# Optimization experiments

Measured on AMD Instinct MI355X. Metric: run time of the kernel, lower is better.

Reference implementation:

```python
import jax, jax.numpy as jnp
import numpy as np

B, T, D_IN, D_OUT, N_HEAD = 2, 2048, 1024, 1024, 16
HEAD_DIM = D_OUT // N_HEAD


def setup_inputs() -> dict:
    key = jax.random.key(0)
    k1, k2, k3, k4 = jax.random.split(key, 4)
    s = 0.02  # init scale for weights
    return {
        "x": jax.random.normal(k1, (B, T, D_IN), jnp.float32),
        "Wq": jax.random.normal(k2, (D_OUT, D_IN), jnp.float32) * s,
        "Wk": jax.random.normal(k3, (D_OUT, D_IN), jnp.float32) * s,
        "Wv": jax.random.normal(k4, (D_OUT, D_IN), jnp.float32) * s,
    }


def reference(x, Wq, Wk, Wv):
    b, t, _ = x.shape
    h, hd = N_HEAD, HEAD_DIM
    # Linear projections (torch Linear: x @ W.T), split heads -> [b,h,t,hd]
    q = (x @ Wq.T).reshape(b, t, h, hd).transpose(0, 2, 1, 3)
    k = (x @ Wk.T).reshape(b, t, h, hd).transpose(0, 2, 1, 3)
    v = (x @ Wv.T).reshape(b, t, h, hd).transpose(0, 2, 1, 3)
    # raw scores [b,h,t,t], causal mask BEFORE scaling (as in source)
    omega = jnp.einsum("bhqd,bhkd->bhqk", q, k)
    causal = jnp.triu(jnp.ones((t, t), dtype=bool), k=1)
    omega = jnp.where(causal, -jnp.inf, omega)
    attw = jax.nn.softmax(omega / jnp.sqrt(jnp.asarray(hd, omega.dtype)), axis=-1)
    ctx = jnp.einsum("bhqk,bhkd->bhqd", attw, v)  # [b,h,t,hd]
    # Faithful to source: transpose(2,3) then view(B,T,d_out)
    out = jnp.swapaxes(ctx, 2, 3).reshape(b, t, D_OUT)
    return out
```

## Files before the change

### kernel.cpp

```cpp
#include <hip/hip_runtime.h>
#include <hip/hip_bf16.h>
#include <stdint.h>

typedef __attribute__((ext_vector_type(8))) short s16x8;
typedef __attribute__((ext_vector_type(4))) float f32x4;

#define T_   2048
#define NH   16
#define HD   64
#define DIN  1024
#define SCALE_LOG2 0.18033688011112042f

#define MFMA32(a, b, c) __builtin_amdgcn_mfma_f32_16x16x32_bf16(a, b, c, 0, 0, 0)

__device__ __forceinline__ unsigned short f2bf(float f) {
  union { float f; uint32_t u; } c; c.f = f;
  uint32_t u = c.u;
  return (unsigned short)((u + 0x7FFFu + ((u >> 16) & 1u)) >> 16);
}

__device__ __forceinline__ uint32_t pk_bf16(float a, float b) {
  __hip_bfloat162 h = __float22bfloat162_rn(make_float2(a, b));
  return *reinterpret_cast<uint32_t*>(&h);
}

#define GLL(gp, lp) __builtin_amdgcn_global_load_lds( \
    (__attribute__((address_space(1))) void*)(gp),    \
    (__attribute__((address_space(3))) void*)(lp), 16, 0, 0)

__global__ __launch_bounds__(256) void cvt_kernel(
    const float* __restrict__ x,  const float* __restrict__ wq,
    const float* __restrict__ wk, const float* __restrict__ wv,
    unsigned short* __restrict__ xb, unsigned short* __restrict__ wb) {
  int i = (blockIdx.x * 256 + threadIdx.x) * 4;
  float4 v;
  unsigned short* dp;
  if (i < 4194304) {
    v = *(const float4*)(x + i);
    dp = xb + i;
  } else {
    int j = i - 4194304;
    int seg = j >> 20, r = j & 1048575;
    const float* w = (seg == 0) ? wq : (seg == 1) ? wk : wv;
    v = *(const float4*)(w + r);
    dp = wb + j;
  }
  ushort4 o;
  o.x = f2bf(v.x); o.y = f2bf(v.y); o.z = f2bf(v.z); o.w = f2bf(v.w);
  *(ushort4*)dp = o;
}

__global__ __launch_bounds__(256) void qkv_gemm(
    const unsigned short* __restrict__ A, const unsigned short* __restrict__ Bm,
    unsigned short* __restrict__ qkv) {
  __shared__ __attribute__((aligned(16))) unsigned short Alds[64 * 64];
  __shared__ __attribute__((aligned(16))) unsigned short Blds[128 * 64];
  const int tid = threadIdx.x;
  const int lane = tid & 63, wave = tid >> 6;
  const int wm = wave >> 1, wn = wave & 1;
  const int m0 = blockIdx.y * 64, n0 = blockIdx.x * 128;

  f32x4 acc[2][4] = {};

  const int srA = wave * 16 + (lane >> 3);
  const int srB = wave * 32 + (lane >> 3);
  const int scol = (((lane & 7) ^ ((lane >> 3) & 7))) * 8;
  const unsigned short* ag = A  + (size_t)(m0 + srA) * DIN + scol;
  const unsigned short* bg = Bm + (size_t)(n0 + srB) * DIN + scol;
  unsigned short* al = &Alds[wave * 16 * 64];
  unsigned short* bl = &Blds[wave * 32 * 64];

  const int l16 = lane & 15, quad = lane >> 4;
  const int sw = l16 & 7;

  for (int k0 = 0; k0 < DIN; k0 += 64) {
    __syncthreads();
#pragma unroll
    for (int i = 0; i < 2; i++)
      GLL(ag + (size_t)i * 8 * DIN + k0, al + i * 512);
#pragma unroll
    for (int i = 0; i < 4; i++)
      GLL(bg + (size_t)i * 8 * DIN + k0, bl + i * 512);
    __syncthreads();
#pragma unroll
    for (int ks = 0; ks < 2; ks++) {
      const int cl = ((ks * 4 + quad) ^ sw) * 8;
      s16x8 af[2], bf[4];
#pragma unroll
      for (int mt = 0; mt < 2; mt++)
        af[mt] = *(const s16x8*)&Alds[(wm * 32 + mt * 16 + l16) * 64 + cl];
#pragma unroll
      for (int nt = 0; nt < 4; nt++)
        bf[nt] = *(const s16x8*)&Blds[(wn * 64 + nt * 16 + l16) * 64 + cl];
#pragma unroll
      for (int mt = 0; mt < 2; mt++)
#pragma unroll
        for (int nt = 0; nt < 4; nt++)
          acc[mt][nt] = MFMA32(af[mt], bf[nt], acc[mt][nt]);
    }
  }

#pragma unroll
  for (int mt = 0; mt < 2; mt++) {
    int mbase = m0 + wm * 32 + mt * 16 + (quad << 2);
    int b = mbase >> 11, t = mbase & 2047;
#pragma unroll
    for (int nt = 0; nt < 4; nt++) {
      int n = n0 + wn * 64 + nt * 16 + l16;
      int sel = n >> 10, h = (n >> 6) & 15, d = n & 63;
      int bh = b * NH + h;
      if (sel == 2) {
        ushort4 pk;
        pk.x = f2bf(acc[mt][nt][0]); pk.y = f2bf(acc[mt][nt][1]);
        pk.z = f2bf(acc[mt][nt][2]); pk.w = f2bf(acc[mt][nt][3]);
        *(ushort4*)&qkv[8388608 + (size_t)(bh * HD + d) * T_ + t] = pk;
      } else {
        float qs = (sel == 0) ? SCALE_LOG2 : 1.f;
#pragma unroll
        for (int r = 0; r < 4; r++)
          qkv[(size_t)sel * 4194304 + (size_t)(bh * T_ + t + r) * HD + d] =
              f2bf(acc[mt][nt][r] * qs);
      }
    }
  }
}

__global__ __launch_bounds__(256) void attn_kernel(
    const unsigned short* __restrict__ qkv, float* __restrict__ out) {
  __shared__ __attribute__((aligned(16))) unsigned short Klds[64 * 64];
  __shared__ __attribute__((aligned(16))) unsigned short Vt[64 * 64];
  __shared__ __attribute__((aligned(16))) unsigned short Plds[64 * 64];

  const int lane = threadIdx.x & 63, wave = threadIdx.x >> 6;
  const int l16 = lane & 15, quad = lane >> 4;
  const int swl = l16 & 7;
  const int qt = 31 - blockIdx.y, bh = blockIdx.x;
  const int q0 = qt * 64;
  const size_t bh_off = (size_t)bh * (T_ * HD);
  const unsigned short* Q  = qkv + bh_off;
  const unsigned short* Kb = qkv + 4194304 + bh_off;
  const unsigned short* Vb = qkv + 8388608 + bh_off;

  s16x8 qf[2];
  {
    const unsigned short* qp =
        Q + (size_t)(q0 + wave * 16 + l16) * HD + quad * 8;
    qf[0] = *(const s16x8*)(qp);
    qf[1] = *(const s16x8*)(qp + 32);
  }

  const int sr = threadIdx.x >> 3;
  const int sc = (threadIdx.x & 7) * 8;
  const int swc = (((threadIdx.x & 7) ^ (sr & 7))) * 8;

  s16x8 kr0 = *(const s16x8*)&Kb[(size_t)sr * HD + sc];
  s16x8 kr1 = *(const s16x8*)&Kb[(size_t)(sr + 32) * HD + sc];
  s16x8 vr0 = *(const s16x8*)&Vb[(size_t)sr * T_ + sc];
  s16x8 vr1 = *(const s16x8*)&Vb[(size_t)(sr + 32) * T_ + sc];

  const s16x8 onesf = {0x3F80, 0x3F80, 0x3F80, 0x3F80,
                       0x3F80, 0x3F80, 0x3F80, 0x3F80};
  f32x4 o[4] = {};
  f32x4 lacc = {};

  uint32_t* prow = (uint32_t*)&Plds[(wave * 16 + l16) * 64];
  const unsigned short* prd = &Plds[(wave * 16 + l16) * 64];

  for (int kt = 0; kt <= qt; kt++) {
    __syncthreads();
    *(s16x8*)&Klds[sr * 64 + swc] = kr0;
    *(s16x8*)&Klds[(sr + 32) * 64 + swc] = kr1;
    *(s16x8*)&Vt[sr * 64 + swc] = vr0;
    *(s16x8*)&Vt[(sr + 32) * 64 + swc] = vr1;
    if (kt < qt) {
      const unsigned short* kp = Kb + (size_t)(kt + 1) * 64 * HD;
      const unsigned short* vp = Vb + (kt + 1) * 64;
      kr0 = *(const s16x8*)&kp[(size_t)sr * HD + sc];
      kr1 = *(const s16x8*)&kp[(size_t)(sr + 32) * HD + sc];
      vr0 = *(const s16x8*)&vp[(size_t)sr * T_ + sc];
      vr1 = *(const s16x8*)&vp[(size_t)(sr + 32) * T_ + sc];
    }
    __syncthreads();

    f32x4 s[4] = {};
#pragma unroll
    for (int kk = 0; kk < 2; kk++) {
      const int cl = ((kk * 4 + quad) ^ swl) * 8;
#pragma unroll
      for (int nt = 0; nt < 4; nt++) {
        s16x8 kf = *(const s16x8*)&Klds[(nt * 16 + l16) * 64 + cl];
        s[nt] = MFMA32(kf, qf[kk], s[nt]);
      }
    }

    if (kt < qt) {
#pragma unroll
      for (int nt = 0; nt < 4; nt++) {
        float p0 = exp2f(s[nt][0]);
        float p1 = exp2f(s[nt][1]);
        float p2 = exp2f(s[nt][2]);
        float p3 = exp2f(s[nt][3]);
        *(uint2*)&prow[(((2 * nt + (quad >> 1)) ^ swl) << 2) + (quad & 1) * 2] =
            make_uint2(pk_bf16(p0, p1), pk_bf16(p2, p3));
      }
    } else {
      const int lim = wave * 16 + l16;
#pragma unroll
      for (int nt = 0; nt < 4; nt++) {
        const int kb = nt * 16 + quad * 4;
        float p0 = (kb + 0 <= lim) ? exp2f(s[nt][0]) : 0.f;
        float p1 = (kb + 1 <= lim) ? exp2f(s[nt][1]) : 0.f;
        float p2 = (kb + 2 <= lim) ? exp2f(s[nt][2]) : 0.f;
        float p3 = (kb + 3 <= lim) ? exp2f(s[nt][3]) : 0.f;
        *(uint2*)&prow[(((2 * nt + (quad >> 1)) ^ swl) << 2) + (quad & 1) * 2] =
            make_uint2(pk_bf16(p0, p1), pk_bf16(p2, p3));
      }
    }

#pragma unroll
    for (int kk = 0; kk < 2; kk++) {
      const int cl = ((kk * 4 + quad) ^ swl) * 8;
      s16x8 pf = *(const s16x8*)&prd[cl];
      lacc = MFMA32(pf, onesf, lacc);
#pragma unroll
      for (int dt = 0; dt < 4; dt++) {
        s16x8 vf = *(const s16x8*)&Vt[(dt * 16 + l16) * 64 + cl];
        o[dt] = MFMA32(pf, vf, o[dt]);
      }
    }
  }

  f32x4 inv;
#pragma unroll
  for (int r = 0; r < 4; r++) inv[r] = 1.f / lacc[r];
#pragma unroll
  for (int dt = 0; dt < 4; dt++) {
    float4 v = make_float4(o[dt][0] * inv[0], o[dt][1] * inv[1],
                           o[dt][2] * inv[2], o[dt][3] * inv[3]);
    *(float4*)(out + (size_t)bh * (HD * T_) + (size_t)(dt * 16 + l16) * T_ +
               q0 + wave * 16 + quad * 4) = v;
  }
}

extern "C" void kernel_launch(void* const* d_in, const int* in_sizes, int n_in,
                              void* d_out, int out_size, void* d_ws, size_t ws_size,
                              hipStream_t stream) {
  const float* x  = (const float*)d_in[0];
  const float* wq = (const float*)d_in[1];
  const float* wk = (const float*)d_in[2];
  const float* wv = (const float*)d_in[3];
  float* out = (float*)d_out;

  unsigned short* xb  = (unsigned short*)d_ws;
  unsigned short* wb  = xb + 4194304;
  unsigned short* qkv = wb + 3145728;

  cvt_kernel<<<7168, 256, 0, stream>>>(x, wq, wk, wv, xb, wb);
  dim3 g1(24, 64);
  qkv_gemm<<<g1, 256, 0, stream>>>(xb, wb, qkv);
  dim3 g2(32, 32);
  attn_kernel<<<g2, 256, 0, stream>>>(qkv, out);
}
```

Measured before the change: 147.3 us.

## Use two waves per 32 query rows with double-buffered direct-to-LDS K/V loads

The attention block drops from four waves to two. Each wave now owns 32 query rows (two 16-row tiles), so every K and V fragment read from LDS feeds two MFMAs. The register-staged K/V prefetch is replaced by asynchronous global-to-LDS loads into a double-buffered K/V tile, which removes one barrier per iteration. In exchange the kernel has fewer waves per block, uses more registers per wave, and relies on the barrier to make the async loads visible before use.

```diff
diff --git a/kernel.cpp b/kernel.cpp
--- a/kernel.cpp
+++ b/kernel.cpp
@@ -125,10 +125,10 @@
   }
 }
 
-__global__ __launch_bounds__(256) void attn_kernel(
+__global__ __launch_bounds__(128) void attn_kernel(
     const unsigned short* __restrict__ qkv, float* __restrict__ out) {
-  __shared__ __attribute__((aligned(16))) unsigned short Klds[64 * 64];
-  __shared__ __attribute__((aligned(16))) unsigned short Vt[64 * 64];
+  __shared__ __attribute__((aligned(16))) unsigned short Klds[2][64 * 64];
+  __shared__ __attribute__((aligned(16))) unsigned short Vt[2][64 * 64];
   __shared__ __attribute__((aligned(16))) unsigned short Plds[64 * 64];
 
   const int lane = threadIdx.x & 63, wave = threadIdx.x >> 6;
@@ -141,104 +141,127 @@
   const unsigned short* Kb = qkv + 4194304 + bh_off;
   const unsigned short* Vb = qkv + 8388608 + bh_off;
 
-  s16x8 qf[2];
-  {
+  s16x8 qf[2][2];
+#pragma unroll
+  for (int nt = 0; nt < 2; nt++) {
     const unsigned short* qp =
-        Q + (size_t)(q0 + wave * 16 + l16) * HD + quad * 8;
-    qf[0] = *(const s16x8*)(qp);
-    qf[1] = *(const s16x8*)(qp + 32);
-  }
-
-  const int sr = threadIdx.x >> 3;
-  const int sc = (threadIdx.x & 7) * 8;
-  const int swc = (((threadIdx.x & 7) ^ (sr & 7))) * 8;
-
-  s16x8 kr0 = *(const s16x8*)&Kb[(size_t)sr * HD + sc];
-  s16x8 kr1 = *(const s16x8*)&Kb[(size_t)(sr + 32) * HD + sc];
-  s16x8 vr0 = *(const s16x8*)&Vb[(size_t)sr * T_ + sc];
-  s16x8 vr1 = *(const s16x8*)&Vb[(size_t)(sr + 32) * T_ + sc];
+        Q + (size_t)(q0 + wave * 32 + nt * 16 + l16) * HD + quad * 8;
+    qf[nt][0] = *(const s16x8*)(qp);
+    qf[nt][1] = *(const s16x8*)(qp + 32);
+  }
+
+  const int r8 = lane >> 3;
+  const int xc = ((lane & 7) ^ r8) * 8;
+  const unsigned short* kg = Kb + (size_t)(wave * 32 + r8) * HD + xc;
+  const unsigned short* vg = Vb + (size_t)(wave * 32 + r8) * T_ + xc;
+  const int sbase = wave * 32 * 64;
 
   const s16x8 onesf = {0x3F80, 0x3F80, 0x3F80, 0x3F80,
                        0x3F80, 0x3F80, 0x3F80, 0x3F80};
-  f32x4 o[4] = {};
-  f32x4 lacc = {};
-
-  uint32_t* prow = (uint32_t*)&Plds[(wave * 16 + l16) * 64];
-  const unsigned short* prd = &Plds[(wave * 16 + l16) * 64];
-
+  f32x4 o[2][4] = {};
+  f32x4 lacc[2] = {};
+
+#pragma unroll
+  for (int i = 0; i < 4; i++) {
+    GLL(kg + (size_t)i * 8 * HD, &Klds[0][sbase + i * 8 * 64]);
+    GLL(vg + (size_t)i * 8 * T_, &Vt[0][sbase + i * 8 * 64]);
+  }
+
+  int cur = 0;
   for (int kt = 0; kt <= qt; kt++) {
     __syncthreads();
-    *(s16x8*)&Klds[sr * 64 + swc] = kr0;
-    *(s16x8*)&Klds[(sr + 32) * 64 + swc] = kr1;
-    *(s16x8*)&Vt[sr * 64 + swc] = vr0;
-    *(s16x8*)&Vt[(sr + 32) * 64 + swc] = vr1;
     if (kt < qt) {
-      const unsigned short* kp = Kb + (size_t)(kt + 1) * 64 * HD;
-      const unsigned short* vp = Vb + (kt + 1) * 64;
-      kr0 = *(const s16x8*)&kp[(size_t)sr * HD + sc];
-      kr1 = *(const s16x8*)&kp[(size_t)(sr + 32) * HD + sc];
-      vr0 = *(const s16x8*)&vp[(size_t)sr * T_ + sc];
-      vr1 = *(const s16x8*)&vp[(size_t)(sr + 32) * T_ + sc];
-    }
-    __syncthreads();
-
-    f32x4 s[4] = {};
+      const unsigned short* kp = kg + (size_t)(kt + 1) * 64 * HD;
+      const unsigned short* vp = vg + (kt + 1) * 64;
+      unsigned short* kd = &Klds[cur ^ 1][sbase];
+      unsigned short* vd = &Vt[cur ^ 1][sbase];
+#pragma unroll
+      for (int i = 0; i < 4; i++) {
+        GLL(kp + (size_t)i * 8 * HD, kd + i * 8 * 64);
+        GLL(vp + (size_t)i * 8 * T_, vd + i * 8 * 64);
+      }
+    }
+
+    f32x4 s[4][2] = {};
 #pragma unroll
     for (int kk = 0; kk < 2; kk++) {
       const int cl = ((kk * 4 + quad) ^ swl) * 8;
 #pragma unroll
-      for (int nt = 0; nt < 4; nt++) {
-        s16x8 kf = *(const s16x8*)&Klds[(nt * 16 + l16) * 64 + cl];
-        s[nt] = MFMA32(kf, qf[kk], s[nt]);
+      for (int mt = 0; mt < 4; mt++) {
+        s16x8 kf = *(const s16x8*)&Klds[cur][(mt * 16 + l16) * 64 + cl];
+#pragma unroll
+        for (int nt = 0; nt < 2; nt++)
+          s[mt][nt] = MFMA32(kf, qf[nt][kk], s[mt][nt]);
       }
     }
 
     if (kt < qt) {
 #pragma unroll
-      for (int nt = 0; nt < 4; nt++) {
-        float p0 = exp2f(s[nt][0]);
-        float p1 = exp2f(s[nt][1]);
-        float p2 = exp2f(s[nt][2]);
-        float p3 = exp2f(s[nt][3]);
-        *(uint2*)&prow[(((2 * nt + (quad >> 1)) ^ swl) << 2) + (quad & 1) * 2] =
-            make_uint2(pk_bf16(p0, p1), pk_bf16(p2, p3));
+      for (int nt = 0; nt < 2; nt++) {
+        uint32_t* prow = (uint32_t*)&Plds[(wave * 32 + nt * 16 + l16) * 64];
+#pragma unroll
+        for (int mt = 0; mt < 4; mt++) {
+          float p0 = exp2f(s[mt][nt][0]);
+          float p1 = exp2f(s[mt][nt][1]);
+          float p2 = exp2f(s[mt][nt][2]);
+          float p3 = exp2f(s[mt][nt][3]);
+          *(uint2*)&prow[(((2 * mt + (quad >> 1)) ^ swl) << 2) +
+                         (quad & 1) * 2] =
+              make_uint2(pk_bf16(p0, p1), pk_bf16(p2, p3));
+        }
       }
     } else {
-      const int lim = wave * 16 + l16;
-#pragma unroll
-      for (int nt = 0; nt < 4; nt++) {
-        const int kb = nt * 16 + quad * 4;
-        float p0 = (kb + 0 <= lim) ? exp2f(s[nt][0]) : 0.f;
-        float p1 = (kb + 1 <= lim) ? exp2f(s[nt][1]) : 0.f;
-        float p2 = (kb + 2 <= lim) ? exp2f(s[nt][2]) : 0.f;
-        float p3 = (kb + 3 <= lim) ? exp2f(s[nt][3]) : 0.f;
-        *(uint2*)&prow[(((2 * nt + (quad >> 1)) ^ swl) << 2) + (quad & 1) * 2] =
-            make_uint2(pk_bf16(p0, p1), pk_bf16(p2, p3));
+#pragma unroll
+      for (int nt = 0; nt < 2; nt++) {
+        const int lim = wave * 32 + nt * 16 + l16;
+        uint32_t* prow = (uint32_t*)&Plds[(wave * 32 + nt * 16 + l16) * 64];
+#pragma unroll
+        for (int mt = 0; mt < 4; mt++) {
+          const int kb = mt * 16 + quad * 4;
+          float p0 = (kb + 0 <= lim) ? exp2f(s[mt][nt][0]) : 0.f;
+          float p1 = (kb + 1 <= lim) ? exp2f(s[mt][nt][1]) : 0.f;
+          float p2 = (kb + 2 <= lim) ? exp2f(s[mt][nt][2]) : 0.f;
+          float p3 = (kb + 3 <= lim) ? exp2f(s[mt][nt][3]) : 0.f;
+          *(uint2*)&prow[(((2 * mt + (quad >> 1)) ^ swl) << 2) +
+                         (quad & 1) * 2] =
+              make_uint2(pk_bf16(p0, p1), pk_bf16(p2, p3));
+        }
       }
     }
 
 #pragma unroll
     for (int kk = 0; kk < 2; kk++) {
       const int cl = ((kk * 4 + quad) ^ swl) * 8;
-      s16x8 pf = *(const s16x8*)&prd[cl];
-      lacc = MFMA32(pf, onesf, lacc);
+      s16x8 pf[2];
+#pragma unroll
+      for (int nt = 0; nt < 2; nt++) {
+        pf[nt] =
+            *(const s16x8*)&Plds[(wave * 32 + nt * 16 + l16) * 64 + cl];
+        lacc[nt] = MFMA32(pf[nt], onesf, lacc[nt]);
+      }
 #pragma unroll
       for (int dt = 0; dt < 4; dt++) {
-        s16x8 vf = *(const s16x8*)&Vt[(dt * 16 + l16) * 64 + cl];
-        o[dt] = MFMA32(pf, vf, o[dt]);
-      }
-    }
-  }
-
-  f32x4 inv;
-#pragma unroll
-  for (int r = 0; r < 4; r++) inv[r] = 1.f / lacc[r];
-#pragma unroll
-  for (int dt = 0; dt < 4; dt++) {
-    float4 v = make_float4(o[dt][0] * inv[0], o[dt][1] * inv[1],
-                           o[dt][2] * inv[2], o[dt][3] * inv[3]);
-    *(float4*)(out + (size_t)bh * (HD * T_) + (size_t)(dt * 16 + l16) * T_ +
-               q0 + wave * 16 + quad * 4) = v;
+        s16x8 vf = *(const s16x8*)&Vt[cur][(dt * 16 + l16) * 64 + cl];
+#pragma unroll
+        for (int nt = 0; nt < 2; nt++)
+          o[nt][dt] = MFMA32(pf[nt], vf, o[nt][dt]);
+      }
+    }
+    cur ^= 1;
+  }
+
+#pragma unroll
+  for (int nt = 0; nt < 2; nt++) {
+    f32x4 inv;
+#pragma unroll
+    for (int r = 0; r < 4; r++) inv[r] = 1.f / lacc[nt][r];
+#pragma unroll
+    for (int dt = 0; dt < 4; dt++) {
+      float4 v = make_float4(o[nt][dt][0] * inv[0], o[nt][dt][1] * inv[1],
+                             o[nt][dt][2] * inv[2], o[nt][dt][3] * inv[3]);
+      *(float4*)(out + (size_t)bh * (HD * T_) + (size_t)(dt * 16 + l16) * T_ +
+                 q0 + wave * 32 + nt * 16 + quad * 4) = v;
+    }
   }
 }
 
@@ -259,5 +282,5 @@
   dim3 g1(24, 64);
   qkv_gemm<<<g1, 256, 0, stream>>>(xb, wb, qkv);
   dim3 g2(32, 32);
-  attn_kernel<<<g2, 256, 0, stream>>>(qkv, out);
-}
+  attn_kernel<<<g2, 128, 0, stream>>>(qkv, out);
+}
```

After: 166.5 us. +13.1%, slower.

## Pair causal query tiles per block to balance attention workload

Applied to the files above, without the earlier changes.

Each attention block now processes two query tiles, a long one (qa = 31-qb) and a short one (qb), streaming the needed K/V tiles for both in a single 33-iteration loop. The grid is halved accordingly. This aims to remove the causal load imbalance where late blocks run 32 tiles and early blocks run 1. In exchange it uses more registers for two sets of accumulators and Q fragments, and has half as many blocks, which could reduce occupancy or latency hiding.

```diff
diff --git a/kernel.cpp b/kernel.cpp
--- a/kernel.cpp
+++ b/kernel.cpp
@@ -125,56 +125,118 @@
   }
 }
 
+__device__ __forceinline__ void tile_step(
+    const unsigned short* Klds, const unsigned short* Vt,
+    unsigned short* Plds, const s16x8 qf0, const s16x8 qf1,
+    f32x4 o[4], f32x4& lacc,
+    const int l16, const int quad, const int swl, const int wave,
+    const bool diag) {
+  f32x4 s[4] = {};
+#pragma unroll
+  for (int kk = 0; kk < 2; kk++) {
+    const int cl = ((kk * 4 + quad) ^ swl) * 8;
+    const s16x8 q = kk ? qf1 : qf0;
+#pragma unroll
+    for (int mt = 0; mt < 4; mt++) {
+      s16x8 kf = *(const s16x8*)&Klds[(mt * 16 + l16) * 64 + cl];
+      s[mt] = MFMA32(kf, q, s[mt]);
+    }
+  }
+
+  uint32_t* prow = (uint32_t*)&Plds[(wave * 16 + l16) * 64];
+  if (!diag) {
+#pragma unroll
+    for (int mt = 0; mt < 4; mt++) {
+      float p0 = exp2f(s[mt][0]);
+      float p1 = exp2f(s[mt][1]);
+      float p2 = exp2f(s[mt][2]);
+      float p3 = exp2f(s[mt][3]);
+      *(uint2*)&prow[(((2 * mt + (quad >> 1)) ^ swl) << 2) + (quad & 1) * 2] =
+          make_uint2(pk_bf16(p0, p1), pk_bf16(p2, p3));
+    }
+  } else {
+    const int lim = wave * 16 + l16;
+#pragma unroll
+    for (int mt = 0; mt < 4; mt++) {
+      const int kb = mt * 16 + quad * 4;
+      float p0 = (kb + 0 <= lim) ? exp2f(s[mt][0]) : 0.f;
+      float p1 = (kb + 1 <= lim) ? exp2f(s[mt][1]) : 0.f;
+      float p2 = (kb + 2 <= lim) ? exp2f(s[mt][2]) : 0.f;
+      float p3 = (kb + 3 <= lim) ? exp2f(s[mt][3]) : 0.f;
+      *(uint2*)&prow[(((2 * mt + (quad >> 1)) ^ swl) << 2) + (quad & 1) * 2] =
+          make_uint2(pk_bf16(p0, p1), pk_bf16(p2, p3));
+    }
+  }
+
+  const s16x8 onesf = {0x3F80, 0x3F80, 0x3F80, 0x3F80,
+                       0x3F80, 0x3F80, 0x3F80, 0x3F80};
+  const unsigned short* prd = &Plds[(wave * 16 + l16) * 64];
+#pragma unroll
+  for (int kk = 0; kk < 2; kk++) {
+    const int cl = ((kk * 4 + quad) ^ swl) * 8;
+    s16x8 pf = *(const s16x8*)&prd[cl];
+    lacc = MFMA32(pf, onesf, lacc);
+#pragma unroll
+    for (int dt = 0; dt < 4; dt++) {
+      s16x8 vf = *(const s16x8*)&Vt[(dt * 16 + l16) * 64 + cl];
+      o[dt] = MFMA32(pf, vf, o[dt]);
+    }
+  }
+}
+
 __global__ __launch_bounds__(256) void attn_kernel(
     const unsigned short* __restrict__ qkv, float* __restrict__ out) {
   __shared__ __attribute__((aligned(16))) unsigned short Klds[64 * 64];
   __shared__ __attribute__((aligned(16))) unsigned short Vt[64 * 64];
   __shared__ __attribute__((aligned(16))) unsigned short Plds[64 * 64];
 
-  const int lane = threadIdx.x & 63, wave = threadIdx.x >> 6;
+  const int tid = threadIdx.x;
+  const int lane = tid & 63, wave = tid >> 6;
   const int l16 = lane & 15, quad = lane >> 4;
   const int swl = l16 & 7;
-  const int qt = 31 - blockIdx.y, bh = blockIdx.x;
-  const int q0 = qt * 64;
+  const int bh = blockIdx.x;
+  const int qb = blockIdx.y;
+  const int qa = 31 - qb;
   const size_t bh_off = (size_t)bh * (T_ * HD);
   const unsigned short* Q  = qkv + bh_off;
   const unsigned short* Kb = qkv + 4194304 + bh_off;
   const unsigned short* Vb = qkv + 8388608 + bh_off;
 
-  s16x8 qf[2];
+  s16x8 qfa0, qfa1, qfb0, qfb1;
   {
     const unsigned short* qp =
-        Q + (size_t)(q0 + wave * 16 + l16) * HD + quad * 8;
-    qf[0] = *(const s16x8*)(qp);
-    qf[1] = *(const s16x8*)(qp + 32);
-  }
-
-  const int sr = threadIdx.x >> 3;
-  const int sc = (threadIdx.x & 7) * 8;
-  const int swc = (((threadIdx.x & 7) ^ (sr & 7))) * 8;
+        Q + (size_t)(qa * 64 + wave * 16 + l16) * HD + quad * 8;
+    qfa0 = *(const s16x8*)(qp);
+    qfa1 = *(const s16x8*)(qp + 32);
+    const unsigned short* qq =
+        Q + (size_t)(qb * 64 + wave * 16 + l16) * HD + quad * 8;
+    qfb0 = *(const s16x8*)(qq);
+    qfb1 = *(const s16x8*)(qq + 32);
+  }
+
+  const int sr = tid >> 3;
+  const int sc = (tid & 7) * 8;
+  const int swc = (((tid & 7) ^ (sr & 7))) * 8;
 
   s16x8 kr0 = *(const s16x8*)&Kb[(size_t)sr * HD + sc];
   s16x8 kr1 = *(const s16x8*)&Kb[(size_t)(sr + 32) * HD + sc];
   s16x8 vr0 = *(const s16x8*)&Vb[(size_t)sr * T_ + sc];
   s16x8 vr1 = *(const s16x8*)&Vb[(size_t)(sr + 32) * T_ + sc];
 
-  const s16x8 onesf = {0x3F80, 0x3F80, 0x3F80, 0x3F80,
-                       0x3F80, 0x3F80, 0x3F80, 0x3F80};
-  f32x4 o[4] = {};
-  f32x4 lacc = {};
-
-  uint32_t* prow = (uint32_t*)&Plds[(wave * 16 + l16) * 64];
-  const unsigned short* prd = &Plds[(wave * 16 + l16) * 64];
-
-  for (int kt = 0; kt <= qt; kt++) {
+  f32x4 oa[4] = {}, ob[4] = {};
+  f32x4 la = {}, lb = {};
+
+  for (int it = 0; it < 33; it++) {
+    const bool pa = (it <= qa);
     __syncthreads();
     *(s16x8*)&Klds[sr * 64 + swc] = kr0;
     *(s16x8*)&Klds[(sr + 32) * 64 + swc] = kr1;
     *(s16x8*)&Vt[sr * 64 + swc] = vr0;
     *(s16x8*)&Vt[(sr + 32) * 64 + swc] = vr1;
-    if (kt < qt) {
-      const unsigned short* kp = Kb + (size_t)(kt + 1) * 64 * HD;
-      const unsigned short* vp = Vb + (kt + 1) * 64;
+    if (it < 32) {
+      const int nk = (it < qa) ? it + 1 : it - qa;
+      const unsigned short* kp = Kb + (size_t)nk * 64 * HD;
+      const unsigned short* vp = Vb + nk * 64;
       kr0 = *(const s16x8*)&kp[(size_t)sr * HD + sc];
       kr1 = *(const s16x8*)&kp[(size_t)(sr + 32) * HD + sc];
       vr0 = *(const s16x8*)&vp[(size_t)sr * T_ + sc];
@@ -182,63 +244,29 @@
     }
     __syncthreads();
 
-    f32x4 s[4] = {};
-#pragma unroll
-    for (int kk = 0; kk < 2; kk++) {
-      const int cl = ((kk * 4 + quad) ^ swl) * 8;
-#pragma unroll
-      for (int nt = 0; nt < 4; nt++) {
-        s16x8 kf = *(const s16x8*)&Klds[(nt * 16 + l16) * 64 + cl];
-        s[nt] = MFMA32(kf, qf[kk], s[nt]);
-      }
-    }
-
-    if (kt < qt) {
-#pragma unroll
-      for (int nt = 0; nt < 4; nt++) {
-        float p0 = exp2f(s[nt][0]);
-        float p1 = exp2f(s[nt][1]);
-        float p2 = exp2f(s[nt][2]);
-        float p3 = exp2f(s[nt][3]);
-        *(uint2*)&prow[(((2 * nt + (quad >> 1)) ^ swl) << 2) + (quad & 1) * 2] =
-            make_uint2(pk_bf16(p0, p1), pk_bf16(p2, p3));
-      }
-    } else {
-      const int lim = wave * 16 + l16;
-#pragma unroll
-      for (int nt = 0; nt < 4; nt++) {
-        const int kb = nt * 16 + quad * 4;
-        float p0 = (kb + 0 <= lim) ? exp2f(s[nt][0]) : 0.f;
-        float p1 = (kb + 1 <= lim) ? exp2f(s[nt][1]) : 0.f;
-        float p2 = (kb + 2 <= lim) ? exp2f(s[nt][2]) : 0.f;
-        float p3 = (kb + 3 <= lim) ? exp2f(s[nt][3]) : 0.f;
-        *(uint2*)&prow[(((2 * nt + (quad >> 1)) ^ swl) << 2) + (quad & 1) * 2] =
-            make_uint2(pk_bf16(p0, p1), pk_bf16(p2, p3));
-      }
-    }
-
-#pragma unroll
-    for (int kk = 0; kk < 2; kk++) {
-      const int cl = ((kk * 4 + quad) ^ swl) * 8;
-      s16x8 pf = *(const s16x8*)&prd[cl];
-      lacc = MFMA32(pf, onesf, lacc);
-#pragma unroll
-      for (int dt = 0; dt < 4; dt++) {
-        s16x8 vf = *(const s16x8*)&Vt[(dt * 16 + l16) * 64 + cl];
-        o[dt] = MFMA32(pf, vf, o[dt]);
-      }
-    }
-  }
-
-  f32x4 inv;
-#pragma unroll
-  for (int r = 0; r < 4; r++) inv[r] = 1.f / lacc[r];
-#pragma unroll
-  for (int dt = 0; dt < 4; dt++) {
-    float4 v = make_float4(o[dt][0] * inv[0], o[dt][1] * inv[1],
-                           o[dt][2] * inv[2], o[dt][3] * inv[3]);
-    *(float4*)(out + (size_t)bh * (HD * T_) + (size_t)(dt * 16 + l16) * T_ +
-               q0 + wave * 16 + quad * 4) = v;
+    if (pa)
+      tile_step(Klds, Vt, Plds, qfa0, qfa1, oa, la, l16, quad, swl, wave,
+                it == qa);
+    else
+      tile_step(Klds, Vt, Plds, qfb0, qfb1, ob, lb, l16, quad, swl, wave,
+                it == 32);
+  }
+
+#pragma unroll
+  for (int half = 0; half < 2; half++) {
+    const f32x4* o = half ? ob : oa;
+    const f32x4 lacc = half ? lb : la;
+    const int q0 = (half ? qb : qa) * 64;
+    f32x4 inv;
+#pragma unroll
+    for (int r = 0; r < 4; r++) inv[r] = 1.f / lacc[r];
+#pragma unroll
+    for (int dt = 0; dt < 4; dt++) {
+      float4 v = make_float4(o[dt][0] * inv[0], o[dt][1] * inv[1],
+                             o[dt][2] * inv[2], o[dt][3] * inv[3]);
+      *(float4*)(out + (size_t)bh * (HD * T_) + (size_t)(dt * 16 + l16) * T_ +
+                 q0 + wave * 16 + quad * 4) = v;
+    }
   }
 }
 
@@ -258,6 +286,6 @@
   cvt_kernel<<<7168, 256, 0, stream>>>(x, wq, wk, wv, xb, wb);
   dim3 g1(24, 64);
   qkv_gemm<<<g1, 256, 0, stream>>>(xb, wb, qkv);
-  dim3 g2(32, 32);
+  dim3 g2(32, 16);
   attn_kernel<<<g2, 256, 0, stream>>>(qkv, out);
 }
```

New measurement: 154.2 us. +4.7%, slower.
